# Kernel optimization log

Measured on AMD Instinct MI355X. Metric: run time of the kernel, lower is better.

Reference implementation:

```python
import jax, jax.numpy as jnp
import numpy as np


def setup_inputs() -> dict:
    key = jax.random.key(0)
    k1, k2 = jax.random.split(key)
    images = jax.random.normal(k1, (32, 512, 32, 32), dtype=jnp.float32)
    atts = jax.random.normal(k2, (32, 512, 512), dtype=jnp.float32)
    return {"images": images, "atts": atts}


def reference(images, atts):
    # Original: softmax over last dim of atts, then broadcast-multiply
    # [N,C,C,H,W] and sum over dim=2 -> equivalent to per-sample matmul:
    # out[n,c,h,w] = sum_d softmax(atts)[n,c,d] * images[n,d,h,w]
    w = jax.nn.softmax(atts, axis=-1)          # [N,C,C]
    return jnp.einsum('ncd,ndhw->nchw', w, images)
```

## Files before the change

kernel.cpp:

```cpp
#include <hip/hip_runtime.h>
#include <stdint.h>

typedef __attribute__((ext_vector_type(4))) float  f32x4;
typedef __attribute__((ext_vector_type(8))) __bf16 bf16x8;

#define NB   32
#define CC   512
#define DD   512
#define HW   1024
#define NKS  16

#define WAITL()  asm volatile("s_waitcnt lgkmcnt(0)" ::: "memory")
#define BARR()   do { asm volatile("" ::: "memory"); __builtin_amdgcn_s_barrier(); \
                      asm volatile("" ::: "memory"); } while (0)

__global__ __launch_bounds__(512, 2) void fused_kernel(
        const float* __restrict__ images, const float* __restrict__ atts,
        float* __restrict__ out) {
    __shared__ unsigned short lA[128][512];
    __shared__ unsigned short lB[8][4][64][8];

    const int b  = blockIdx.x;
    const int g  = b & 7;
    const int q  = b >> 3;
    const int n  = (q & 3) * 8 + g;
    const int t  = q >> 2;
    const int rt = t & 3;
    const int ct = t >> 2;

    const int tid  = threadIdx.x;
    const int lane = tid & 63;
    const int w    = tid >> 6;
    const int r15  = lane & 15;
    const int kgl  = lane >> 4;

    const float* gAt = atts + (size_t)n * CC * DD + (size_t)(rt * 128) * DD;
    const float* gB  = images + (size_t)n * DD * HW + ct * 512 + w * 64;
    float*       gO  = out + (size_t)n * CC * HW + (size_t)(rt * 128) * HW
                           + ct * 512 + w * 64;

    {
        const int grp = tid >> 4;
        const int l16 = tid & 15;
        for (int s = 0; s < 4; ++s) {
            const int row = grp * 4 + s;
            const float* ap = gAt + (size_t)row * DD;
            f32x4 v[8];
            #pragma unroll
            for (int p = 0; p < 4; ++p) {
                v[2*p]   = *(const f32x4*)(ap + (p * 16 + l16) * 8);
                v[2*p+1] = *(const f32x4*)(ap + (p * 16 + l16) * 8 + 4);
            }
            float m = v[0][0];
            #pragma unroll
            for (int j = 0; j < 8; ++j)
                #pragma unroll
                for (int c = 0; c < 4; ++c) m = fmaxf(m, v[j][c]);
            #pragma unroll
            for (int k = 1; k < 16; k <<= 1) m = fmaxf(m, __shfl_xor(m, k, 16));
            float sum = 0.f;
            #pragma unroll
            for (int j = 0; j < 8; ++j)
                #pragma unroll
                for (int c = 0; c < 4; ++c) {
                    v[j][c] = __expf(v[j][c] - m);
                    sum += v[j][c];
                }
            #pragma unroll
            for (int k = 1; k < 16; k <<= 1) sum += __shfl_xor(sum, k, 16);
            const float inv = 1.0f / sum;
            #pragma unroll
            for (int p = 0; p < 4; ++p) {
                bf16x8 wv;
                #pragma unroll
                for (int e = 0; e < 8; ++e)
                    wv[e] = (__bf16)(v[2*p + (e >> 2)][e & 3] * inv);
                const int slot = (p * 16 + l16) ^ (row & 7);
                *(bf16x8*)&lA[row][slot * 8] = wv;
            }
        }
    }
    WAITL();
    BARR();

    f32x4 acc[8][4] = {};
    f32x4 bA[8], bB[8];

    auto loadB = [&](int kt, f32x4 (&d)[8]) {
        const float* p = gB + (size_t)(kt * 32 + kgl * 8) * HW + r15 * 4;
        #pragma unroll
        for (int j = 0; j < 8; ++j)
            d[j] = *(const f32x4*)(p + (size_t)j * HW);
    };
    auto writeB = [&](const f32x4 (&d)[8]) {
        #pragma unroll
        for (int cc = 0; cc < 4; ++cc) {
            bf16x8 wv;
            #pragma unroll
            for (int j = 0; j < 8; ++j) wv[j] = (__bf16)d[j][cc];
            const int slot = cc * 16 + (r15 ^ (cc << 2));
            *(bf16x8*)&lB[w][kgl][slot][0] = wv;
        }
    };
    auto compute = [&](int kt) {
        bf16x8 af[8], bv[4];
        #pragma unroll
        for (int m = 0; m < 8; ++m) {
            const int slot = ((kt << 2) + kgl) ^ (r15 & 7);
            af[m] = *(const bf16x8*)&lA[m * 16 + r15][slot * 8];
        }
        #pragma unroll
        for (int nf = 0; nf < 4; ++nf) {
            const int c    = nf * 16 + r15;
            const int slot = (c & 3) * 16 + (((c >> 2) ^ ((c & 3) << 2)) & 15);
            bv[nf] = *(const bf16x8*)&lB[w][kgl][slot][0];
        }
        #pragma unroll
        for (int m = 0; m < 8; ++m)
            #pragma unroll
            for (int nf = 0; nf < 4; ++nf)
                acc[m][nf] = __builtin_amdgcn_mfma_f32_16x16x32_bf16(
                    af[m], bv[nf], acc[m][nf], 0, 0, 0);
    };

    loadB(0, bA);
    loadB(1, bB);
    writeB(bA);
    #pragma unroll
    for (int kt = 0; kt < NKS; ++kt) {
        compute(kt);
        if (kt + 1 < NKS) {
            if (kt & 1) {
                writeB(bA);
                if (kt + 2 < NKS) loadB(kt + 2, bB);
            } else {
                writeB(bB);
                if (kt + 2 < NKS) loadB(kt + 2, bA);
            }
        }
    }

    #pragma unroll
    for (int m = 0; m < 8; ++m)
        #pragma unroll
        for (int nf = 0; nf < 4; ++nf)
            #pragma unroll
            for (int r = 0; r < 4; ++r) {
                const int row = m * 16 + kgl * 4 + r;
                const int col = nf * 16 + r15;
                gO[(size_t)row * HW + col] = acc[m][nf][r];
            }
}

extern "C" void kernel_launch(void* const* d_in, const int* in_sizes, int n_in,
                              void* d_out, int out_size, void* d_ws, size_t ws_size,
                              hipStream_t stream) {
    const float* images = (const float*)d_in[0];
    const float* atts   = (const float*)d_in[1];
    float*       out    = (float*)d_out;

    fused_kernel<<<dim3(NB * 8), dim3(512), 0, stream>>>(images, atts, out);
}
```

Baseline: 35.92 us.

## Overlap B prefetch and LDS writes with softmax and MFMA work

The softmax prologue now handles two attention rows per iteration, so more global loads are in flight at once. The first two image-tile loads are issued before the barrier, which hides their latency behind the softmax tail. In the main loop, each warp reads its B fragments from LDS, writes the next tile, and only then runs the MFMAs, so the LDS store overlaps matrix work. The cost is higher register pressure under the 512x2 launch bounds, which could cause spills.

```diff
diff --git a/kernel.cpp b/kernel.cpp
--- a/kernel.cpp
+++ b/kernel.cpp
@@ -39,51 +39,6 @@
     float*       gO  = out + (size_t)n * CC * HW + (size_t)(rt * 128) * HW
                            + ct * 512 + w * 64;
 
-    {
-        const int grp = tid >> 4;
-        const int l16 = tid & 15;
-        for (int s = 0; s < 4; ++s) {
-            const int row = grp * 4 + s;
-            const float* ap = gAt + (size_t)row * DD;
-            f32x4 v[8];
-            #pragma unroll
-            for (int p = 0; p < 4; ++p) {
-                v[2*p]   = *(const f32x4*)(ap + (p * 16 + l16) * 8);
-                v[2*p+1] = *(const f32x4*)(ap + (p * 16 + l16) * 8 + 4);
-            }
-            float m = v[0][0];
-            #pragma unroll
-            for (int j = 0; j < 8; ++j)
-                #pragma unroll
-                for (int c = 0; c < 4; ++c) m = fmaxf(m, v[j][c]);
-            #pragma unroll
-            for (int k = 1; k < 16; k <<= 1) m = fmaxf(m, __shfl_xor(m, k, 16));
-            float sum = 0.f;
-            #pragma unroll
-            for (int j = 0; j < 8; ++j)
-                #pragma unroll
-                for (int c = 0; c < 4; ++c) {
-                    v[j][c] = __expf(v[j][c] - m);
-                    sum += v[j][c];
-                }
-            #pragma unroll
-            for (int k = 1; k < 16; k <<= 1) sum += __shfl_xor(sum, k, 16);
-            const float inv = 1.0f / sum;
-            #pragma unroll
-            for (int p = 0; p < 4; ++p) {
-                bf16x8 wv;
-                #pragma unroll
-                for (int e = 0; e < 8; ++e)
-                    wv[e] = (__bf16)(v[2*p + (e >> 2)][e & 3] * inv);
-                const int slot = (p * 16 + l16) ^ (row & 7);
-                *(bf16x8*)&lA[row][slot * 8] = wv;
-            }
-        }
-    }
-    WAITL();
-    BARR();
-
-    f32x4 acc[8][4] = {};
     f32x4 bA[8], bB[8];
 
     auto loadB = [&](int kt, f32x4 (&d)[8]) {
@@ -92,6 +47,68 @@
         for (int j = 0; j < 8; ++j)
             d[j] = *(const f32x4*)(p + (size_t)j * HW);
     };
+
+    {
+        const int grp = tid >> 4;
+        const int l16 = tid & 15;
+        #pragma unroll
+        for (int s = 0; s < 4; s += 2) {
+            const int row0 = grp * 4 + s;
+            const int row1 = row0 + 1;
+            const float* ap0 = gAt + (size_t)row0 * DD;
+            const float* ap1 = gAt + (size_t)row1 * DD;
+            f32x4 v0[8], v1[8];
+            #pragma unroll
+            for (int p = 0; p < 4; ++p) {
+                v0[2*p]   = *(const f32x4*)(ap0 + (p * 16 + l16) * 8);
+                v0[2*p+1] = *(const f32x4*)(ap0 + (p * 16 + l16) * 8 + 4);
+            }
+            #pragma unroll
+            for (int p = 0; p < 4; ++p) {
+                v1[2*p]   = *(const f32x4*)(ap1 + (p * 16 + l16) * 8);
+                v1[2*p+1] = *(const f32x4*)(ap1 + (p * 16 + l16) * 8 + 4);
+            }
+            #pragma unroll
+            for (int rr = 0; rr < 2; ++rr) {
+                f32x4 (&v)[8] = rr ? v1 : v0;
+                const int row = rr ? row1 : row0;
+                float m = v[0][0];
+                #pragma unroll
+                for (int j = 0; j < 8; ++j)
+                    #pragma unroll
+                    for (int c = 0; c < 4; ++c) m = fmaxf(m, v[j][c]);
+                #pragma unroll
+                for (int k = 1; k < 16; k <<= 1) m = fmaxf(m, __shfl_xor(m, k, 16));
+                float sum = 0.f;
+                #pragma unroll
+                for (int j = 0; j < 8; ++j)
+                    #pragma unroll
+                    for (int c = 0; c < 4; ++c) {
+                        v[j][c] = __expf(v[j][c] - m);
+                        sum += v[j][c];
+                    }
+                #pragma unroll
+                for (int k = 1; k < 16; k <<= 1) sum += __shfl_xor(sum, k, 16);
+                const float inv = 1.0f / sum;
+                #pragma unroll
+                for (int p = 0; p < 4; ++p) {
+                    bf16x8 wv;
+                    #pragma unroll
+                    for (int e = 0; e < 8; ++e)
+                        wv[e] = (__bf16)(v[2*p + (e >> 2)][e & 3] * inv);
+                    const int slot = (p * 16 + l16) ^ (row & 7);
+                    *(bf16x8*)&lA[row][slot * 8] = wv;
+                }
+            }
+        }
+    }
+    loadB(0, bA);
+    loadB(1, bB);
+    WAITL();
+    BARR();
+
+    f32x4 acc[8][4] = {};
+
     auto writeB = [&](const f32x4 (&d)[8]) {
         #pragma unroll
         for (int cc = 0; cc < 4; ++cc) {
@@ -102,18 +119,20 @@
             *(bf16x8*)&lB[w][kgl][slot][0] = wv;
         }
     };
-    auto compute = [&](int kt) {
-        bf16x8 af[8], bv[4];
-        #pragma unroll
-        for (int m = 0; m < 8; ++m) {
-            const int slot = ((kt << 2) + kgl) ^ (r15 & 7);
-            af[m] = *(const bf16x8*)&lA[m * 16 + r15][slot * 8];
-        }
+    auto readBv = [&](bf16x8 (&bv)[4]) {
         #pragma unroll
         for (int nf = 0; nf < 4; ++nf) {
             const int c    = nf * 16 + r15;
             const int slot = (c & 3) * 16 + (((c >> 2) ^ ((c & 3) << 2)) & 15);
             bv[nf] = *(const bf16x8*)&lB[w][kgl][slot][0];
+        }
+    };
+    auto computeA = [&](int kt, const bf16x8 (&bv)[4]) {
+        bf16x8 af[8];
+        #pragma unroll
+        for (int m = 0; m < 8; ++m) {
+            const int slot = ((kt << 2) + kgl) ^ (r15 & 7);
+            af[m] = *(const bf16x8*)&lA[m * 16 + r15][slot * 8];
         }
         #pragma unroll
         for (int m = 0; m < 8; ++m)
@@ -123,12 +142,11 @@
                     af[m], bv[nf], acc[m][nf], 0, 0, 0);
     };
 
-    loadB(0, bA);
-    loadB(1, bB);
     writeB(bA);
     #pragma unroll
     for (int kt = 0; kt < NKS; ++kt) {
-        compute(kt);
+        bf16x8 bv[4];
+        readBv(bv);
         if (kt + 1 < NKS) {
             if (kt & 1) {
                 writeB(bA);
@@ -138,6 +156,7 @@
                 if (kt + 2 < NKS) loadB(kt + 2, bA);
             }
         }
+        computeA(kt, bv);
     }
 
     #pragma unroll
```

Measured after the change: 38.26 us. +6.5%, slower.
